# Performance work log

Hardware: AMD Instinct MI355X
Metric: run time of the kernel (lower is better)

Reference implementation:

```python
import jax, jax.numpy as jnp
import numpy as np
from jax import lax

B, N, CIN, COUT = 8, 4096, 64, 128
S, NS, V = 1024, 32, 4
RADIUS = 0.2
H1, H2 = 64, 128
BN_EPS = 1e-5


def _fps(xyz, n_sample):
    # farthest point sampling, deterministic start at index 0
    Bb, Nn, _ = xyz.shape
    start = jnp.zeros((Bb,), jnp.int32)
    mind0 = jnp.full((Bb, Nn), jnp.inf, xyz.dtype)

    def body(carry, _):
        mind, last = carry
        p = jnp.take_along_axis(xyz, last[:, None, None], axis=1)  # [B,1,3]
        d = jnp.sum((xyz - p) ** 2, -1)                             # [B,N]
        mind = jnp.minimum(mind, d)
        nxt = jnp.argmax(mind, -1).astype(jnp.int32)
        return (mind, nxt), nxt

    (_, _), rest = lax.scan(body, (mind0, start), None, length=n_sample - 1)
    idx = jnp.concatenate([start[None], rest], 0).T                 # [B,S]
    new_xyz = jnp.take_along_axis(xyz, idx[..., None], axis=1)      # [B,S,3]
    return new_xyz, idx


def _ball_query_idx(new_xyz, xyz, K, radius):
    # first K points (in index order) within radius, padded with -1
    d2 = jnp.sum((new_xyz[:, :, None, :] - xyz[:, None, :, :]) ** 2, -1)  # [B,S,N]
    within = d2 < radius * radius
    Nn = xyz.shape[1]
    ar = jnp.arange(Nn)
    key = jnp.where(within, ar, Nn + ar)            # in-ball points sort first, stably by index
    sel = jnp.argsort(key, axis=-1)[:, :, :K]       # [B,S,K]
    valid = jnp.take_along_axis(within, sel, axis=-1)
    return jnp.where(valid, sel, -1)


def _masked_gather(f, idx):
    # gather rows of f [B,N,C] with idx (any batched shape); idx==-1 -> zeros
    mask = idx == -1
    safe = jnp.where(mask, 0, idx)
    g = jax.vmap(lambda fb, ib: fb[ib])(f, safe)
    return jnp.where(mask[..., None], jnp.zeros((), f.dtype), g)


def _bn(x, gamma, beta, axes):
    # training-mode batchnorm over `axes` (channel is last dim)
    mu = jnp.mean(x, axes, keepdims=True)
    var = jnp.mean((x - mu) ** 2, axes, keepdims=True)
    return (x - mu) * (gamma / jnp.sqrt(var + BN_EPS)) + beta


def setup_inputs() -> dict:
    key = jax.random.key(0)
    ks = jax.random.split(key, 16)
    sc = 0.05
    inp = {
        "xyz": jax.random.uniform(ks[0], (B, N, 3), jnp.float32),
        "f": jax.random.normal(ks[1], (B, N, CIN), jnp.float32),
        "centroid_idx": jax.random.randint(ks[2], (V,), 0, NS),
        "affine_weight": jnp.ones((CIN + 6,), jnp.float32),
        "affine_bias": jnp.zeros((CIN + 6,), jnp.float32),
        "mix_w": sc * jax.random.normal(ks[3], (CIN, 2 * CIN + 6), jnp.float32),
        "mix_b": jnp.zeros((CIN,), jnp.float32),
        "m1_w1": sc * jax.random.normal(ks[4], (H1, 13), jnp.float32),
        "m1_b1": jnp.zeros((H1,), jnp.float32),
        "m1_g1": jnp.ones((H1,), jnp.float32),
        "m1_be1": jnp.zeros((H1,), jnp.float32),
        "m1_w2": sc * jax.random.normal(ks[5], (CIN, H1), jnp.float32),
        "m1_b2": jnp.zeros((CIN,), jnp.float32),
        "m2_w1": sc * jax.random.normal(ks[6], (H2, CIN), jnp.float32),
        "m2_b1": jnp.zeros((H2,), jnp.float32),
        "m2_g1": jnp.ones((H2,), jnp.float32),
        "m2_be1": jnp.zeros((H2,), jnp.float32),
        "m2_w2": sc * jax.random.normal(ks[7], (COUT, H2), jnp.float32),
        "m2_b2": jnp.zeros((COUT,), jnp.float32),
        "res_w": sc * jax.random.normal(ks[8], (COUT, CIN), jnp.float32),
        "res_b": jnp.zeros((COUT,), jnp.float32),
    }
    return inp


def reference(xyz, f, centroid_idx, affine_weight, affine_bias, mix_w, mix_b,
              m1_w1, m1_b1, m1_g1, m1_be1, m1_w2, m1_b2,
              m2_w1, m2_b1, m2_g1, m2_be1, m2_w2, m2_b2, res_w, res_b):
    Bb = xyz.shape[0]
    # ---- Grouping ----
    new_xyz, new_idx = _fps(xyz, S)                     # [B,S,3], [B,S]
    gidx = _ball_query_idx(new_xyz, xyz, NS, RADIUS)    # [B,S,n]
    mask = gidx == -1
    grouped_xyz = _masked_gather(xyz, gidx)             # [B,S,n,3]
    grouped_feat = _masked_gather(f, gidx)              # [B,S,n,cin]
    sampled = _masked_gather(f, new_idx)[:, :, None, :]  # [B,S,1,cin]
    gxl = grouped_xyz - new_xyz[:, :, None, :]
    gfl = grouped_feat - sampled
    gf = jnp.concatenate([grouped_xyz, gxl, gfl], -1)   # [B,S,n,cin+6]
    std = jnp.std(gf.reshape(Bb, -1), axis=-1, ddof=1).reshape(Bb, 1, 1, 1)
    gf = gf / (std + 1e-5)
    gf = affine_weight * gf + affine_bias
    gf = jnp.concatenate([gf, jnp.broadcast_to(sampled, (Bb, S, NS, CIN))], -1)
    grouped_f = jnp.einsum('bsnc,oc->bsno', gf, mix_w) + mix_b  # [B,S,n,cin]
    group_skip = grouped_f

    # ---- multi-centroid relative geometry (rel_jk, 13 channels) ----
    mc = xyz[:, centroid_idx, :]                                       # [B,V,3]
    arrow = grouped_xyz[:, :, :, None, :] - mc[:, None, None, :, :]    # [B,S,n,V,3]
    eu = jnp.sqrt(jnp.sum(arrow ** 2, -1, keepdims=True))              # [B,S,n,V,1]
    gx_b = jnp.broadcast_to(grouped_xyz[:, :, :, None, :], arrow.shape)
    mc_b = jnp.broadcast_to(mc[:, None, None, :, :], arrow.shape)
    rel = jnp.concatenate([-arrow, arrow, eu, gx_b, mc_b], -1)         # [B,S,n,V,13]

    # ---- m1: 1x1x1 Conv3d -> BN3d -> GELU -> Conv3d ----
    h = jnp.einsum('bsnvc,oc->bsnvo', rel, m1_w1) + m1_b1
    h = _bn(h, m1_g1, m1_be1, (0, 1, 2, 3))
    h = jax.nn.gelu(h, approximate=False)
    w_jk = jnp.einsum('bsnvc,oc->bsnvo', h, m1_w2) + m1_b2             # [B,S,n,V,cin]

    # ---- gumbel-softmax weighted aggregation over V centroids ----
    logits = grouped_f[:, :, :, None, :] * w_jk                        # [B,S,n,V,cin]
    u = jax.random.uniform(jax.random.key(42), logits.shape, logits.dtype, 1e-9, 1.0)
    gumbel = -jnp.log(-jnp.log(u))
    soft_w = jax.nn.softmax(logits + gumbel, axis=3)  # softmax over V (tau=1, soft)
    agg = jnp.sum(soft_w * logits, axis=3)                             # [B,S,n,cin]
    agg = agg + group_skip
    agg = jnp.where(mask[..., None], jnp.zeros((), agg.dtype), agg)

    # ---- m2: 1x1 Conv2d -> BN2d -> Conv2d, residual, max-pool over n ----
    h2 = jnp.einsum('bsnc,oc->bsno', agg, m2_w1) + m2_b1
    h2 = _bn(h2, m2_g1, m2_be1, (0, 1, 2))
    out = jnp.einsum('bsnc,oc->bsno', h2, m2_w2) + m2_b2               # [B,S,n,cout]
    res = jnp.einsum('bsnc,oc->bsno', group_skip, res_w) + res_b
    new_f = jax.nn.gelu(out + res, approximate=False)
    new_f = jnp.max(new_f, axis=2)                                     # [B,S,cout]
    return new_f, new_xyz
```

## Files before the change

kernel.cpp:

```cpp
#include <hip/hip_runtime.h>
#include <cstdint>
#include <cstddef>

#define TF_PARTITIONABLE 1

constexpr int B_ = 8, N_ = 4096, CIN_ = 64, COUT_ = 128;
constexpr int S_ = 1024, NS_ = 32, V_ = 4;
constexpr int ROWS_ = B_ * S_ * NS_;

constexpr size_t OFF_ACC   = 0;
constexpr size_t ACC_BYTES = 35072;
constexpr size_t OFF_SCALE = 35072;
constexpr size_t OFF_W1P   = 35328;
constexpr size_t OFF_B1P   = 38656;
constexpr size_t OFF_WCOMB = 38912;
constexpr size_t OFF_BCOMB = 71680;
constexpr size_t OFF_MIXWT = 72192;
constexpr size_t OFF_NIDX  = 106496;
constexpr size_t OFF_GIDX  = 139264;
constexpr size_t OFF_GF    = 1187840;
constexpr size_t OFF_AGG   = 68296704;

constexpr int AC_BATCH = 0;
constexpr int AC_G     = 16;
constexpr int AC_E     = 88;
constexpr int AC_S2A   = 216;
constexpr int AC_M2    = 280;

__device__ __forceinline__ float gelu_f(float x) {
    return 0.5f * x * (1.0f + erff(x * 0.7071067811865476f));
}

#define TF_ROUND(r) { x0 += x1; x1 = (x1 << (r)) | (x1 >> (32 - (r))); x1 ^= x0; }

__device__ __forceinline__ unsigned tf_random_bits(unsigned lo) {
    const unsigned ks0 = 0u, ks1 = 42u, ks2 = 0x1BD11BDAu ^ 0u ^ 42u;
#if TF_PARTITIONABLE
    unsigned x0 = 0u + ks0, x1 = lo + ks1;
#else
    unsigned j = lo & 0x01FFFFFFu;
    unsigned x0 = j + ks0, x1 = (j + 0x02000000u) + ks1;
#endif
    TF_ROUND(13) TF_ROUND(15) TF_ROUND(26) TF_ROUND(6)
    x0 += ks1; x1 += ks2 + 1u;
    TF_ROUND(17) TF_ROUND(29) TF_ROUND(16) TF_ROUND(24)
    x0 += ks2; x1 += ks0 + 2u;
    TF_ROUND(13) TF_ROUND(15) TF_ROUND(26) TF_ROUND(6)
    x0 += ks0; x1 += ks1 + 3u;
    TF_ROUND(17) TF_ROUND(29) TF_ROUND(16) TF_ROUND(24)
    x0 += ks1; x1 += ks2 + 4u;
    TF_ROUND(13) TF_ROUND(15) TF_ROUND(26) TF_ROUND(6)
    x0 += ks2; x1 += ks0 + 5u;
#if TF_PARTITIONABLE
    return x0 ^ x1;
#else
    return (lo < 0x02000000u) ? x0 : x1;
#endif
}

__device__ __forceinline__ float gumbel_from_bits(unsigned bits) {
    float fl = __uint_as_float((bits >> 9) | 0x3f800000u) - 1.0f;
    float u  = fmaxf(1e-9f, fl + 1e-9f);
    return -logf(-logf(u));
}

__device__ __forceinline__ float wsum(float v) {
    for (int o = 32; o; o >>= 1) v += __shfl_down(v, o);
    return v;
}

__global__ __launch_bounds__(256) void k_fps(const float* __restrict__ xyz,
                                             int* __restrict__ new_idx,
                                             float* __restrict__ new_xyz) {
    __shared__ float sx[4096], sy[4096], sz[4096];
    __shared__ __align__(16) float swv[2][4];
    __shared__ __align__(16) int   swi[2][4];
    int b = blockIdx.x, t = threadIdx.x, lane = t & 63, wid = t >> 6;
    const float* xb = xyz + (size_t)b * 12288;
    float px[16], py[16], pz[16], md[16];
    int i0 = t * 16;
#pragma unroll
    for (int j = 0; j < 16; j++) {
        int i = i0 + j;
        float x = xb[i * 3], y = xb[i * 3 + 1], z = xb[i * 3 + 2];
        px[j] = x; py[j] = y; pz[j] = z;
        sx[i] = x; sy[i] = y; sz[i] = z;
        md[j] = __builtin_inff();
    }
    __syncthreads();
    float cx = sx[0], cy = sy[0], cz = sz[0];
    if (t == 0) {
        new_idx[b * 1024] = 0;
        new_xyz[(size_t)b * 3072 + 0] = cx;
        new_xyz[(size_t)b * 3072 + 1] = cy;
        new_xyz[(size_t)b * 3072 + 2] = cz;
    }
    int p = 0;
    for (int it = 1; it < 1024; ++it) {
        float bv = -1.0f; int bj = 0;
#pragma unroll
        for (int j = 0; j < 16; j++) {
            float dx = __fsub_rn(px[j], cx), dy = __fsub_rn(py[j], cy), dz = __fsub_rn(pz[j], cz);
            float d = __fadd_rn(__fadd_rn(__fmul_rn(dx, dx), __fmul_rn(dy, dy)), __fmul_rn(dz, dz));
            float m2 = fminf(md[j], d); md[j] = m2;
            if (m2 > bv) { bv = m2; bj = j; }
        }
        int bi = i0 + bj;
        float mx = bv;
#pragma unroll
        for (int off = 1; off < 64; off <<= 1) mx = fmaxf(mx, __shfl_xor(mx, off));
        unsigned long long msk = __ballot(bv == mx);
        int winlane = __ffsll(msk) - 1;
        int wbi = __shfl(bi, winlane);
        if (lane == 0) { swv[p][wid] = mx; swi[p][wid] = wbi; }
        __syncthreads();
        float4 vv = *(const float4*)&swv[p][0];
        int4   ii4 = *(const int4*)&swi[p][0];
        float best = vv.x; int ii = ii4.x;
        if (vv.y > best) { best = vv.y; ii = ii4.y; }
        if (vv.z > best) { best = vv.z; ii = ii4.z; }
        if (vv.w > best) { best = vv.w; ii = ii4.w; }
        cx = sx[ii]; cy = sy[ii]; cz = sz[ii];
        if (t == 0) {
            new_idx[b * 1024 + it] = ii;
            size_t o3 = ((size_t)b * 1024 + it) * 3;
            new_xyz[o3] = cx; new_xyz[o3 + 1] = cy; new_xyz[o3 + 2] = cz;
        }
        p ^= 1;
    }
}

__global__ __launch_bounds__(256) void k_ball(const float* __restrict__ xyz,
                                              const float* __restrict__ new_xyz,
                                              int* __restrict__ gidx) {
    int gw = blockIdx.x * 4 + (threadIdx.x >> 6);
    int lane = threadIdx.x & 63;
    int b = gw >> 10;
    const float* xb = xyz + (size_t)b * 12288;
    float qx = new_xyz[gw * 3], qy = new_xyz[gw * 3 + 1], qz = new_xyz[gw * 3 + 2];
    int* out = gidx + (size_t)gw * 32;
    int have = 0;
    for (int c0 = 0; c0 < 4096; c0 += 64) {
        int i = c0 + lane;
        float dx = __fsub_rn(qx, xb[i * 3]);
        float dy = __fsub_rn(qy, xb[i * 3 + 1]);
        float dz = __fsub_rn(qz, xb[i * 3 + 2]);
        float d2 = __fadd_rn(__fadd_rn(__fmul_rn(dx, dx), __fmul_rn(dy, dy)), __fmul_rn(dz, dz));
        bool within = d2 < 0.04f;
        unsigned long long mv = __ballot(within);
        int rank = __popcll(mv & ((1ull << lane) - 1ull));
        int pos = have + rank;
        if (within && pos < 32) out[pos] = i;
        have += (int)__popcll(mv);
        if (have >= 32) break;
    }
    for (int j = have + lane; j < 32; j += 64) out[j] = -1;
}

__global__ __launch_bounds__(256) void k_stats(const float* __restrict__ xyz,
                                               const float* __restrict__ f,
                                               const int* __restrict__ cidx,
                                               const int* __restrict__ new_idx,
                                               const int* __restrict__ gidx,
                                               const float* __restrict__ new_xyz,
                                               double* __restrict__ acc) {
    int b = blockIdx.x >> 5, blk = blockIdx.x & 31;
    int t = threadIdx.x, lane = t & 63;
    const float* xb = xyz + (size_t)b * 12288;
    const float* fb = f + ((size_t)b << 18);
    float mc[4][3];
#pragma unroll
    for (int v = 0; v < 4; v++) {
        int ci = cidx[v];
        mc[v][0] = xb[ci * 3]; mc[v][1] = xb[ci * 3 + 1]; mc[v][2] = xb[ci * 3 + 2];
    }
    float sum = 0.f, ssq = 0.f;
    float G1x = 0, G1y = 0, G1z = 0, Gxx = 0, Gxy = 0, Gxz = 0, Gyy = 0, Gyz = 0, Gzz = 0;
    float E1[4] = {0, 0, 0, 0}, Eax[4] = {0, 0, 0, 0}, Eay[4] = {0, 0, 0, 0}, Eaz[4] = {0, 0, 0, 0};
    for (int rr = 0; rr < 4; ++rr) {
        int row = blk * 1024 + rr * 256 + t;
        int s = row >> 5;
        int gi = gidx[((size_t)b << 15) + row];
        bool msk = gi < 0;
        int sg = (b << 10) + s;
        float nx = new_xyz[sg * 3], ny = new_xyz[sg * 3 + 1], nz = new_xyz[sg * 3 + 2];
        int nid = new_idx[sg];
        float gx = 0, gy = 0, gz = 0;
        if (!msk) { gx = xb[gi * 3]; gy = xb[gi * 3 + 1]; gz = xb[gi * 3 + 2]; }
        float a3 = __fsub_rn(gx, nx), a4 = __fsub_rn(gy, ny), a5 = __fsub_rn(gz, nz);
        sum += gx + gy + gz + a3 + a4 + a5;
        ssq += gx * gx + gy * gy + gz * gz + a3 * a3 + a4 * a4 + a5 * a5;
        const float4* fsp = (const float4*)(fb + ((size_t)nid << 6));
        int gi0 = msk ? 0 : gi;
        const float4* fip = (const float4*)(fb + ((size_t)gi0 << 6));
#pragma unroll
        for (int c4 = 0; c4 < 16; c4++) {
            float4 fs4 = fsp[c4];
            float4 fi4 = fip[c4];
            if (msk) { fi4.x = 0; fi4.y = 0; fi4.z = 0; fi4.w = 0; }
            float d0 = __fsub_rn(fi4.x, fs4.x), d1 = __fsub_rn(fi4.y, fs4.y);
            float d2 = __fsub_rn(fi4.z, fs4.z), d3 = __fsub_rn(fi4.w, fs4.w);
            sum += d0 + d1 + d2 + d3;
            ssq += d0 * d0 + d1 * d1 + d2 * d2 + d3 * d3;
        }
        G1x += gx; G1y += gy; G1z += gz;
        Gxx += gx * gx; Gxy += gx * gy; Gxz += gx * gz;
        Gyy += gy * gy; Gyz += gy * gz; Gzz += gz * gz;
#pragma unroll
        for (int v = 0; v < 4; v++) {
            float ax = __fsub_rn(gx, mc[v][0]), ay = __fsub_rn(gy, mc[v][1]), az = __fsub_rn(gz, mc[v][2]);
            float e = __fsqrt_rn(ax * ax + ay * ay + az * az);
            E1[v] += e; Eax[v] += e * gx; Eay[v] += e * gy; Eaz[v] += e * gz;
        }
    }
    sum = wsum(sum); ssq = wsum(ssq);
    G1x = wsum(G1x); G1y = wsum(G1y); G1z = wsum(G1z);
    Gxx = wsum(Gxx); Gxy = wsum(Gxy); Gxz = wsum(Gxz);
    Gyy = wsum(Gyy); Gyz = wsum(Gyz); Gzz = wsum(Gzz);
#pragma unroll
    for (int v = 0; v < 4; v++) {
        E1[v] = wsum(E1[v]); Eax[v] = wsum(Eax[v]); Eay[v] = wsum(Eay[v]); Eaz[v] = wsum(Eaz[v]);
    }
    if (lane == 0) {
        atomicAdd(&acc[AC_BATCH + b * 2 + 0], (double)sum);
        atomicAdd(&acc[AC_BATCH + b * 2 + 1], (double)ssq);
        double* Gb = acc + AC_G + b * 9;
        atomicAdd(&Gb[0], (double)G1x); atomicAdd(&Gb[1], (double)G1y); atomicAdd(&Gb[2], (double)G1z);
        atomicAdd(&Gb[3], (double)Gxx); atomicAdd(&Gb[4], (double)Gxy); atomicAdd(&Gb[5], (double)Gxz);
        atomicAdd(&Gb[6], (double)Gyy); atomicAdd(&Gb[7], (double)Gyz); atomicAdd(&Gb[8], (double)Gzz);
#pragma unroll
        for (int v = 0; v < 4; v++) {
            double* Eb = acc + AC_E + (b * 4 + v) * 4;
            atomicAdd(&Eb[0], (double)E1[v]);
            atomicAdd(&Eb[1], (double)Eax[v]);
            atomicAdd(&Eb[2], (double)Eay[v]);
            atomicAdd(&Eb[3], (double)Eaz[v]);
        }
    }
}

struct GS { double G1[3]; double G2[6]; double E1; double Ea[3]; double m[3]; };

__device__ __forceinline__ int g2i(int x, int y) {
    if (x > y) { int tt = x; x = y; y = tt; }
    return (x == 0) ? y : ((x == 1) ? (2 + y) : 5);
}

__device__ double pairsum(const GS& g, int ki, int ai, int kj, int aj) {
    const double R = 32768.0;
    if (ki > kj) { int tk = ki; ki = kj; kj = tk; int ta = ai; ai = aj; aj = ta; }
    switch (ki * 4 + kj) {
        case 0:  return g.G2[g2i(ai, aj)] - g.m[ai] * g.G1[aj] - g.m[aj] * g.G1[ai] + R * g.m[ai] * g.m[aj];
        case 1:  return g.Ea[ai] - g.m[ai] * g.E1;
        case 2:  return g.G2[g2i(ai, aj)] - g.m[ai] * g.G1[aj];
        case 3:  return (g.G1[ai] - R * g.m[ai]) * g.m[aj];
        case 5:  { double s = 0; for (int x = 0; x < 3; x++) s += g.G2[g2i(x, x)] - 2.0 * g.m[x] * g.G1[x] + R * g.m[x] * g.m[x]; return s; }
        case 6:  return g.Ea[aj];
        case 7:  return g.E1 * g.m[aj];
        case 10: return g.G2[g2i(ai, aj)];
        case 11: return g.G1[ai] * g.m[aj];
        case 15: return R * g.m[ai] * g.m[aj];
    }
    return 0.0;
}

__device__ __forceinline__ void chdec(int ch, int& kind, int& ax, double& sgn) {
    if (ch < 3)      { kind = 0; ax = ch;      sgn = -1.0; }
    else if (ch < 6) { kind = 0; ax = ch - 3;  sgn = 1.0; }
    else if (ch == 6){ kind = 1; ax = 0;       sgn = 1.0; }
    else if (ch < 10){ kind = 2; ax = ch - 7;  sgn = 1.0; }
    else             { kind = 3; ax = ch - 10; sgn = 1.0; }
}

__device__ GS load_gs(const double* acc, const float* xyz, const int* cidx, int grp) {
    GS g; int b = grp >> 2, v = grp & 3;
    const double* Gb = acc + AC_G + b * 9;
    g.G1[0] = Gb[0]; g.G1[1] = Gb[1]; g.G1[2] = Gb[2];
    for (int q = 0; q < 6; q++) g.G2[q] = Gb[3 + q];
    const double* Eb = acc + AC_E + grp * 4;
    g.E1 = Eb[0]; g.Ea[0] = Eb[1]; g.Ea[1] = Eb[2]; g.Ea[2] = Eb[3];
    int ci = cidx[v];
    g.m[0] = (double)xyz[(size_t)b * 12288 + ci * 3];
    g.m[1] = (double)xyz[(size_t)b * 12288 + ci * 3 + 1];
    g.m[2] = (double)xyz[(size_t)b * 12288 + ci * 3 + 2];
    return g;
}

__global__ __launch_bounds__(256) void k_prep(const double* __restrict__ acc,
                                              const float* __restrict__ xyz,
                                              const int* __restrict__ cidx,
                                              const float* __restrict__ m1w1,
                                              const float* __restrict__ m1b1,
                                              const float* __restrict__ m1g1,
                                              const float* __restrict__ m1be1,
                                              const float* __restrict__ mixw,
                                              float* __restrict__ scale,
                                              float* __restrict__ w1p,
                                              float* __restrict__ b1p,
                                              float* __restrict__ mixwt) {
    __shared__ double Sec[169];
    __shared__ double S1[13];
    int t = threadIdx.x;
    if (t < 8) {
        double sm = acc[AC_BATCH + t * 2], sq = acc[AC_BATCH + t * 2 + 1];
        double M = 2293760.0;
        double var = (sq - sm * sm / M) / (M - 1.0);
        float stdv = (float)sqrt(var);
        scale[t] = 1.0f / (stdv + 1e-5f);
    }
    for (int idx = t; idx < 8576; idx += 256) {
        int k = idx >> 6, o = idx & 63;
        mixwt[idx] = mixw[o * 134 + k];
    }
    if (t < 169) {
        int i = t / 13, j = t % 13;
        int ki, ai, kj, aj; double si, sj;
        chdec(i, ki, ai, si); chdec(j, kj, aj, sj);
        double val = 0;
        for (int grp = 0; grp < 32; grp++) {
            GS g = load_gs(acc, xyz, cidx, grp);
            val += si * sj * pairsum(g, ki, ai, kj, aj);
        }
        Sec[t] = val;
    } else if (t < 182) {
        int i = t - 169;
        int ki, ai; double si;
        chdec(i, ki, ai, si);
        double val = 0;
        const double R = 32768.0;
        for (int grp = 0; grp < 32; grp++) {
            GS g = load_gs(acc, xyz, cidx, grp);
            double tv;
            switch (ki) {
                case 0:  tv = si * (g.G1[ai] - R * g.m[ai]); break;
                case 1:  tv = g.E1; break;
                case 2:  tv = g.G1[ai]; break;
                default: tv = R * g.m[ai]; break;
            }
            val += tv;
        }
        S1[i] = val;
    }
    __syncthreads();
    if (t < 64) {
        double w[13];
        for (int k = 0; k < 13; k++) w[k] = (double)m1w1[t * 13 + k];
        double s1w = 0;
        for (int k = 0; k < 13; k++) s1w += w[k] * S1[k];
        double quad = 0;
        for (int i = 0; i < 13; i++) {
            double s = 0;
            for (int j = 0; j < 13; j++) s += Sec[i * 13 + j] * w[j];
            quad += w[i] * s;
        }
        double M1d = 1048576.0;
        double b1o = (double)m1b1[t];
        double mu = s1w / M1d + b1o;
        double E2 = (quad + 2.0 * b1o * s1w) / M1d + b1o * b1o;
        double var = E2 - mu * mu;
        double gg = (double)m1g1[t] / sqrt(var + 1e-5);
        for (int k = 0; k < 13; k++) w1p[t * 13 + k] = (float)(w[k] * gg);
        b1p[t] = (float)((b1o - mu) * gg + (double)m1be1[t]);
    }
}

__global__ __launch_bounds__(256) void k_groupedf(const float* __restrict__ xyz,
                                                  const float* __restrict__ f,
                                                  const int* __restrict__ new_idx,
                                                  const int* __restrict__ gidx,
                                                  const float* __restrict__ new_xyz,
                                                  const float* __restrict__ scale_p,
                                                  const float* __restrict__ aw,
                                                  const float* __restrict__ ab,
                                                  const float* __restrict__ mixwt,
                                                  const float* __restrict__ mixb,
                                                  float* __restrict__ gf) {
    int r = blockIdx.x * 256 + threadIdx.x;
    int b = r >> 15;
    int rb = r & 32767;
    int s = rb >> 5;
    int gi = gidx[r];
    bool msk = gi < 0;
    int gi0 = msk ? 0 : gi;
    int sg = (b << 10) + s;
    int nid = new_idx[sg];
    float scale = scale_p[b];
    float nx = new_xyz[sg * 3], ny = new_xyz[sg * 3 + 1], nz = new_xyz[sg * 3 + 2];
    const float* xb = xyz + (size_t)b * 12288;
    const float* fb = f + ((size_t)b << 18);
    float gx = 0, gy = 0, gz = 0;
    if (!msk) { gx = xb[gi * 3]; gy = xb[gi * 3 + 1]; gz = xb[gi * 3 + 2]; }
    float acc[64];
#pragma unroll
    for (int o = 0; o < 64; o++) acc[o] = mixb[o];
    float va[6];
    va[0] = gx; va[1] = gy; va[2] = gz;
    va[3] = __fsub_rn(gx, nx); va[4] = __fsub_rn(gy, ny); va[5] = __fsub_rn(gz, nz);
#pragma unroll
    for (int k = 0; k < 6; k++) {
        float g = aw[k] * (va[k] * scale) + ab[k];
        const float* wt = mixwt + k * 64;
#pragma unroll
        for (int o = 0; o < 64; o++) acc[o] += g * wt[o];
    }
    const float4* fip = (const float4*)(fb + ((size_t)gi0 << 6));
    const float4* fsp = (const float4*)(fb + ((size_t)nid << 6));
    for (int c4 = 0; c4 < 16; c4++) {
        float4 fi = fip[c4];
        if (msk) { fi.x = 0; fi.y = 0; fi.z = 0; fi.w = 0; }
        float4 fs4 = fsp[c4];
        float dv[4] = {__fsub_rn(fi.x, fs4.x), __fsub_rn(fi.y, fs4.y),
                       __fsub_rn(fi.z, fs4.z), __fsub_rn(fi.w, fs4.w)};
#pragma unroll
        for (int u = 0; u < 4; u++) {
            int k = 6 + c4 * 4 + u;
            float g = aw[k] * (dv[u] * scale) + ab[k];
            const float* wt = mixwt + k * 64;
#pragma unroll
            for (int o = 0; o < 64; o++) acc[o] += g * wt[o];
        }
    }
    for (int c4 = 0; c4 < 16; c4++) {
        float4 fs4 = fsp[c4];
        float sv[4] = {fs4.x, fs4.y, fs4.z, fs4.w};
#pragma unroll
        for (int u = 0; u < 4; u++) {
            int k = 70 + c4 * 4 + u;
            const float* wt = mixwt + k * 64;
#pragma unroll
            for (int o = 0; o < 64; o++) acc[o] += sv[u] * wt[o];
        }
    }
    float4* dst = (float4*)(gf + ((size_t)r << 6));
#pragma unroll
    for (int c4 = 0; c4 < 16; c4++)
        dst[c4] = make_float4(acc[c4 * 4], acc[c4 * 4 + 1], acc[c4 * 4 + 2], acc[c4 * 4 + 3]);
}

__global__ __launch_bounds__(256) void k_fused(const float* __restrict__ xyz,
                                               const int* __restrict__ cidx,
                                               const int* __restrict__ gidx,
                                               const float* __restrict__ gf,
                                               const float* __restrict__ w1p,
                                               const float* __restrict__ b1p,
                                               const float* __restrict__ w2,
                                               const float* __restrict__ b2,
                                               float* __restrict__ agg) {
    __shared__ float sh[4][4][64];
    __shared__ float smc[4][3];
    int t = threadIdx.x, wv = t >> 6, lane = t & 63;
    int row0 = blockIdx.x * 64;
    int b = row0 >> 15;
    if (t < 12) {
        int v = t / 3, j = t % 3;
        smc[v][j] = xyz[(size_t)b * 12288 + cidx[v] * 3 + j];
    }
    float w1l[13];
#pragma unroll
    for (int k = 0; k < 13; k++) w1l[k] = w1p[lane * 13 + k];
    float b1l = b1p[lane], b2l = b2[lane];
    float w2r[64];
#pragma unroll
    for (int c4 = 0; c4 < 16; c4++) {
        float4 tmp = *(const float4*)(w2 + lane * 64 + c4 * 4);
        w2r[c4 * 4] = tmp.x; w2r[c4 * 4 + 1] = tmp.y; w2r[c4 * 4 + 2] = tmp.z; w2r[c4 * 4 + 3] = tmp.w;
    }
    __syncthreads();
    float mcl[4][3];
#pragma unroll
    for (int v = 0; v < 4; v++) { mcl[v][0] = smc[v][0]; mcl[v][1] = smc[v][1]; mcl[v][2] = smc[v][2]; }
    int r = row0 + wv * 16;
    for (int rr = 0; rr < 16; ++rr, ++r) {
        int gi = gidx[r];
        bool msk = gi < 0;
        float gx = 0, gy = 0, gz = 0;
        if (!msk) {
            const float* p = xyz + (size_t)b * 12288 + (size_t)gi * 3;
            gx = p[0]; gy = p[1]; gz = p[2];
        }
        float gfo = gf[((size_t)r << 6) + lane];
#pragma unroll
        for (int v = 0; v < 4; v++) {
            float ax = __fsub_rn(gx, mcl[v][0]);
            float ay = __fsub_rn(gy, mcl[v][1]);
            float az = __fsub_rn(gz, mcl[v][2]);
            float eu = __fsqrt_rn(__fadd_rn(__fadd_rn(__fmul_rn(ax, ax), __fmul_rn(ay, ay)), __fmul_rn(az, az)));
            float h = b1l
                - ax * w1l[0] - ay * w1l[1] - az * w1l[2]
                + ax * w1l[3] + ay * w1l[4] + az * w1l[5]
                + eu * w1l[6] + gx * w1l[7] + gy * w1l[8] + gz * w1l[9]
                + mcl[v][0] * w1l[10] + mcl[v][1] * w1l[11] + mcl[v][2] * w1l[12];
            sh[wv][v][lane] = gelu_f(h);
        }
        __syncthreads();
        float lg[4];
#pragma unroll
        for (int v = 0; v < 4; v++) {
            float a = b2l;
            const float4* hp = (const float4*)sh[wv][v];
#pragma unroll
            for (int c4 = 0; c4 < 16; c4++) {
                float4 hh = hp[c4];
                a += hh.x * w2r[c4 * 4] + hh.y * w2r[c4 * 4 + 1] + hh.z * w2r[c4 * 4 + 2] + hh.w * w2r[c4 * 4 + 3];
            }
            lg[v] = gfo * a;
        }
        __syncthreads();
        unsigned base = ((unsigned)r << 8) + (unsigned)lane;
        float z0 = lg[0] + gumbel_from_bits(tf_random_bits(base));
        float z1 = lg[1] + gumbel_from_bits(tf_random_bits(base + 64u));
        float z2 = lg[2] + gumbel_from_bits(tf_random_bits(base + 128u));
        float z3 = lg[3] + gumbel_from_bits(tf_random_bits(base + 192u));
        float mx = fmaxf(fmaxf(z0, z1), fmaxf(z2, z3));
        float e0 = __expf(z0 - mx), e1 = __expf(z1 - mx), e2 = __expf(z2 - mx), e3 = __expf(z3 - mx);
        float inv = 1.0f / (e0 + e1 + e2 + e3);
        float av = (e0 * lg[0] + e1 * lg[1] + e2 * lg[2] + e3 * lg[3]) * inv + gfo;
        agg[((size_t)r << 6) + lane] = msk ? 0.0f : av;
    }
}

__global__ __launch_bounds__(256) void k_syrk(const float* __restrict__ agg,
                                              double* __restrict__ acc) {
    __shared__ float As[128][64];
    int t = threadIdx.x;
    int ti = t >> 4, tj = t & 15;
    float C[4][4] = {};
    float cs = 0.f;
    size_t base = (size_t)blockIdx.x * 1024 * 64;
    for (int tile = 0; tile < 8; ++tile) {
        const float4* src = (const float4*)(agg + base + (size_t)tile * 128 * 64);
#pragma unroll
        for (int i = 0; i < 8; i++) {
            int idx = t + i * 256;
            ((float4*)As)[idx] = src[idx];
        }
        __syncthreads();
        for (int rr = 0; rr < 128; ++rr) {
            float4 a = *(const float4*)&As[rr][ti * 4];
            float4 bb = *(const float4*)&As[rr][tj * 4];
            C[0][0] += a.x * bb.x; C[0][1] += a.x * bb.y; C[0][2] += a.x * bb.z; C[0][3] += a.x * bb.w;
            C[1][0] += a.y * bb.x; C[1][1] += a.y * bb.y; C[1][2] += a.y * bb.z; C[1][3] += a.y * bb.w;
            C[2][0] += a.z * bb.x; C[2][1] += a.z * bb.y; C[2][2] += a.z * bb.z; C[2][3] += a.z * bb.w;
            C[3][0] += a.w * bb.x; C[3][1] += a.w * bb.y; C[3][2] += a.w * bb.z; C[3][3] += a.w * bb.w;
            if (t < 64) cs += As[rr][t];
        }
        __syncthreads();
    }
    double* M2 = acc + AC_M2;
#pragma unroll
    for (int i = 0; i < 4; i++)
#pragma unroll
        for (int j = 0; j < 4; j++)
            atomicAdd(&M2[(ti * 4 + i) * 64 + (tj * 4 + j)], (double)C[i][j]);
    if (t < 64) atomicAdd(&acc[AC_S2A + t], (double)cs);
}

__global__ __launch_bounds__(256) void k_comb(const double* __restrict__ acc,
                                              const float* __restrict__ m2w1,
                                              const float* __restrict__ m2b1,
                                              const float* __restrict__ m2g1,
                                              const float* __restrict__ m2be1,
                                              const float* __restrict__ m2w2,
                                              const float* __restrict__ m2b2,
                                              float* __restrict__ wcomb,
                                              float* __restrict__ bcomb) {
    __shared__ float W1s[128 * 64];
    __shared__ float g2s[128], ofss[128];
    int t = threadIdx.x;
    const double* S2a = acc + AC_S2A;
    const double* M2 = acc + AC_M2;
    if (t < 128) {
        float wf[64];
        for (int c = 0; c < 64; c++) wf[c] = m2w1[t * 64 + c];
        double sw = 0;
        for (int c = 0; c < 64; c++) sw += (double)wf[c] * S2a[c];
        double quad = 0;
        for (int i = 0; i < 64; i++) {
            double s = 0;
            for (int j = 0; j < 64; j++) s += (double)wf[j] * M2[i * 64 + j];
            quad += (double)wf[i] * s;
        }
        double Rd = 262144.0;
        double b1o = (double)m2b1[t];
        double mu = sw / Rd + b1o;
        double E2 = (quad + 2.0 * b1o * sw) / Rd + b1o * b1o;
        double var = E2 - mu * mu;
        double gg = (double)m2g1[t] / sqrt(var + 1e-5);
        g2s[t] = (float)gg;
        ofss[t] = (float)(((double)m2b1[t] - mu) * gg + (double)m2be1[t]);
    }
    __syncthreads();
    for (int idx = t; idx < 128 * 64; idx += 256) {
        int c = idx >> 6, k = idx & 63;
        W1s[idx] = g2s[c] * m2w1[c * 64 + k];
    }
    __syncthreads();
    for (int idx = t; idx < 128 * 64; idx += 256) {
        int o = idx >> 6, k = idx & 63;
        float s = 0;
        for (int c = 0; c < 128; c++) s += m2w2[o * 128 + c] * W1s[c * 64 + k];
        wcomb[idx] = s;
    }
    if (t < 128) {
        float s = m2b2[t];
        for (int c = 0; c < 128; c++) s += m2w2[t * 128 + c] * ofss[c];
        bcomb[t] = s;
    }
}

__global__ __launch_bounds__(256) void k_final(const float* __restrict__ agg,
                                               const float* __restrict__ gf,
                                               const float* __restrict__ wcomb,
                                               const float* __restrict__ bcomb,
                                               const float* __restrict__ resw,
                                               const float* __restrict__ resb,
                                               float* __restrict__ out_f) {
    __shared__ float rbuf[8][128];
    int t = threadIdx.x, wv = t >> 6, lane = t & 63;
    int which = lane >> 5, n = lane & 31;
    int gw = blockIdx.x * 8 + wv * 2 + which;
    size_t r = (size_t)gw * 32 + n;
    float ar[64], sk[64];
    const float4* ap = (const float4*)(agg + (r << 6));
    const float4* sp = (const float4*)(gf + (r << 6));
#pragma unroll
    for (int c4 = 0; c4 < 16; c4++) {
        float4 x = ap[c4];
        ar[c4 * 4] = x.x; ar[c4 * 4 + 1] = x.y; ar[c4 * 4 + 2] = x.z; ar[c4 * 4 + 3] = x.w;
        float4 y = sp[c4];
        sk[c4 * 4] = y.x; sk[c4 * 4 + 1] = y.y; sk[c4 * 4 + 2] = y.z; sk[c4 * 4 + 3] = y.w;
    }
    for (int o = 0; o < 128; o++) {
        float a1 = bcomb[o], a2 = resb[o];
        const float* wc = wcomb + o * 64;
        const float* rw = resw + o * 64;
#pragma unroll
        for (int c = 0; c < 64; c++) { a1 += ar[c] * wc[c]; a2 += sk[c] * rw[c]; }
        float g = gelu_f(a1 + a2);
#pragma unroll
        for (int off = 16; off; off >>= 1) g = fmaxf(g, __shfl_xor(g, off));
        if (n == 0) rbuf[wv * 2 + which][o] = g;
    }
    __syncthreads();
    int base = blockIdx.x * 8;
    for (int i = t; i < 1024; i += 256) {
        int lr = i >> 7, o = i & 127;
        out_f[(size_t)(base + lr) * 128 + o] = rbuf[lr][o];
    }
}

extern "C" void kernel_launch(void* const* d_in, const int* in_sizes, int n_in,
                              void* d_out, int out_size, void* d_ws, size_t ws_size,
                              hipStream_t stream) {
    (void)in_sizes; (void)n_in; (void)out_size; (void)ws_size;
    const float* xyz  = (const float*)d_in[0];
    const float* f    = (const float*)d_in[1];
    const int*   cidx = (const int*)d_in[2];
    const float* aw   = (const float*)d_in[3];
    const float* ab   = (const float*)d_in[4];
    const float* mixw = (const float*)d_in[5];
    const float* mixb = (const float*)d_in[6];
    const float* m1w1 = (const float*)d_in[7];
    const float* m1b1 = (const float*)d_in[8];
    const float* m1g1 = (const float*)d_in[9];
    const float* m1be1= (const float*)d_in[10];
    const float* m1w2 = (const float*)d_in[11];
    const float* m1b2 = (const float*)d_in[12];
    const float* m2w1 = (const float*)d_in[13];
    const float* m2b1 = (const float*)d_in[14];
    const float* m2g1 = (const float*)d_in[15];
    const float* m2be1= (const float*)d_in[16];
    const float* m2w2 = (const float*)d_in[17];
    const float* m2b2 = (const float*)d_in[18];
    const float* resw = (const float*)d_in[19];
    const float* resb = (const float*)d_in[20];

    float* out_f   = (float*)d_out;
    float* out_xyz = out_f + (size_t)B_ * S_ * COUT_;

    char* ws = (char*)d_ws;
    double* acc  = (double*)(ws + OFF_ACC);
    float* scale = (float*)(ws + OFF_SCALE);
    float* w1p   = (float*)(ws + OFF_W1P);
    float* b1p   = (float*)(ws + OFF_B1P);
    float* wcomb = (float*)(ws + OFF_WCOMB);
    float* bcomb = (float*)(ws + OFF_BCOMB);
    float* mixwt = (float*)(ws + OFF_MIXWT);
    int*   nidx  = (int*)(ws + OFF_NIDX);
    int*   gidx  = (int*)(ws + OFF_GIDX);
    float* gf    = (float*)(ws + OFF_GF);
    float* agg   = (float*)(ws + OFF_AGG);

    hipMemsetAsync(ws, 0, ACC_BYTES, stream);
    hipLaunchKernelGGL(k_fps,      dim3(8),    dim3(256),  0, stream, xyz, nidx, out_xyz);
    hipLaunchKernelGGL(k_ball,     dim3(2048), dim3(256),  0, stream, xyz, out_xyz, gidx);
    hipLaunchKernelGGL(k_stats,    dim3(256),  dim3(256),  0, stream, xyz, f, cidx, nidx, gidx, out_xyz, acc);
    hipLaunchKernelGGL(k_prep,     dim3(1),    dim3(256),  0, stream, acc, xyz, cidx, m1w1, m1b1, m1g1, m1be1, mixw, scale, w1p, b1p, mixwt);
    hipLaunchKernelGGL(k_groupedf, dim3(1024), dim3(256),  0, stream, xyz, f, nidx, gidx, out_xyz, scale, aw, ab, mixwt, mixb, gf);
    hipLaunchKernelGGL(k_fused,    dim3(4096), dim3(256),  0, stream, xyz, cidx, gidx, gf, w1p, b1p, m1w2, m1b2, agg);
    hipLaunchKernelGGL(k_syrk,     dim3(256),  dim3(256),  0, stream, agg, acc);
    hipLaunchKernelGGL(k_comb,     dim3(1),    dim3(256),  0, stream, acc, m2w1, m2b1, m2g1, m2be1, m2w2, m2b2, wcomb, bcomb);
    hipLaunchKernelGGL(k_final,    dim3(1024), dim3(256),  0, stream, agg, gf, wcomb, bcomb, resw, resb, out_f);
}
```

Before: 2.236 ms.

## Speed up FPS wave reduction with DPP, fast erf/log, drop block barriers

Several unrelated changes. The FPS argmax reduction now uses DPP row operations plus readlane instead of shfl_xor butterflies, and the point coordinates are packed into a float4 shared array so each centroid fetch is a single load. GELU uses a polynomial erf approximation (Abramowitz-Stegun), the outer log in the Gumbel noise uses __logf, and two __syncthreads in the per-row aggregation loop are removed because each wave only touches its own shared slice. The approximations may shift numerics, and dropping the barriers assumes no cross-wave sharing and relies on wave-level ordering for the LDS reuse.

```diff
diff --git a/kernel.cpp b/kernel.cpp
--- a/kernel.cpp
+++ b/kernel.cpp
@@ -27,8 +27,17 @@
 constexpr int AC_S2A   = 216;
 constexpr int AC_M2    = 280;
 
+__device__ __forceinline__ float erf_fast(float x) {
+    float ax = fabsf(x);
+    float t = 1.0f / (1.0f + 0.3275911f * ax);
+    float y = t * (0.254829592f + t * (-0.284496736f + t * (1.421413741f +
+              t * (-1.453152027f + t * 1.061405429f))));
+    float r = 1.0f - y * __expf(-ax * ax);
+    return copysignf(r, x);
+}
+
 __device__ __forceinline__ float gelu_f(float x) {
-    return 0.5f * x * (1.0f + erff(x * 0.7071067811865476f));
+    return 0.5f * x * (1.0f + erf_fast(x * 0.7071067811865476f));
 }
 
 #define TF_ROUND(r) { x0 += x1; x1 = (x1 << (r)) | (x1 >> (32 - (r))); x1 ^= x0; }
@@ -61,7 +70,8 @@
 __device__ __forceinline__ float gumbel_from_bits(unsigned bits) {
     float fl = __uint_as_float((bits >> 9) | 0x3f800000u) - 1.0f;
     float u  = fmaxf(1e-9f, fl + 1e-9f);
-    return -logf(-logf(u));
+    float w = -logf(u);
+    return -__logf(w);
 }
 
 __device__ __forceinline__ float wsum(float v) {
@@ -69,10 +79,27 @@
     return v;
 }
 
+__device__ __forceinline__ float wave_max64_nonneg(float v) {
+    int x;
+    x = __builtin_amdgcn_update_dpp(0, __float_as_int(v), 0xB1, 0xf, 0xf, true);
+    v = fmaxf(v, __int_as_float(x));
+    x = __builtin_amdgcn_update_dpp(0, __float_as_int(v), 0x4E, 0xf, 0xf, true);
+    v = fmaxf(v, __int_as_float(x));
+    x = __builtin_amdgcn_update_dpp(0, __float_as_int(v), 0x141, 0xf, 0xf, true);
+    v = fmaxf(v, __int_as_float(x));
+    x = __builtin_amdgcn_update_dpp(0, __float_as_int(v), 0x140, 0xf, 0xf, true);
+    v = fmaxf(v, __int_as_float(x));
+    x = __builtin_amdgcn_update_dpp(0, __float_as_int(v), 0x142, 0xf, 0xf, true);
+    v = fmaxf(v, __int_as_float(x));
+    x = __builtin_amdgcn_update_dpp(0, __float_as_int(v), 0x143, 0xf, 0xf, true);
+    v = fmaxf(v, __int_as_float(x));
+    return __int_as_float(__builtin_amdgcn_readlane(__float_as_int(v), 63));
+}
+
 __global__ __launch_bounds__(256) void k_fps(const float* __restrict__ xyz,
                                              int* __restrict__ new_idx,
                                              float* __restrict__ new_xyz) {
-    __shared__ float sx[4096], sy[4096], sz[4096];
+    __shared__ __align__(16) float4 sxyz[4096];
     __shared__ __align__(16) float swv[2][4];
     __shared__ __align__(16) int   swi[2][4];
     int b = blockIdx.x, t = threadIdx.x, lane = t & 63, wid = t >> 6;
@@ -84,11 +111,12 @@
         int i = i0 + j;
         float x = xb[i * 3], y = xb[i * 3 + 1], z = xb[i * 3 + 2];
         px[j] = x; py[j] = y; pz[j] = z;
-        sx[i] = x; sy[i] = y; sz[i] = z;
+        sxyz[i] = make_float4(x, y, z, 0.0f);
         md[j] = __builtin_inff();
     }
     __syncthreads();
-    float cx = sx[0], cy = sy[0], cz = sz[0];
+    float4 c0 = sxyz[0];
+    float cx = c0.x, cy = c0.y, cz = c0.z;
     if (t == 0) {
         new_idx[b * 1024] = 0;
         new_xyz[(size_t)b * 3072 + 0] = cx;
@@ -105,14 +133,10 @@
             float m2 = fminf(md[j], d); md[j] = m2;
             if (m2 > bv) { bv = m2; bj = j; }
         }
-        int bi = i0 + bj;
-        float mx = bv;
-#pragma unroll
-        for (int off = 1; off < 64; off <<= 1) mx = fmaxf(mx, __shfl_xor(mx, off));
+        float mx = wave_max64_nonneg(bv);
         unsigned long long msk = __ballot(bv == mx);
         int winlane = __ffsll(msk) - 1;
-        int wbi = __shfl(bi, winlane);
-        if (lane == 0) { swv[p][wid] = mx; swi[p][wid] = wbi; }
+        if (lane == winlane) { swv[p][wid] = bv; swi[p][wid] = i0 + bj; }
         __syncthreads();
         float4 vv = *(const float4*)&swv[p][0];
         int4   ii4 = *(const int4*)&swi[p][0];
@@ -120,7 +144,8 @@
         if (vv.y > best) { best = vv.y; ii = ii4.y; }
         if (vv.z > best) { best = vv.z; ii = ii4.z; }
         if (vv.w > best) { best = vv.w; ii = ii4.w; }
-        cx = sx[ii]; cy = sy[ii]; cz = sz[ii];
+        float4 cw = sxyz[ii];
+        cx = cw.x; cy = cw.y; cz = cw.z;
         if (t == 0) {
             new_idx[b * 1024 + it] = ii;
             size_t o3 = ((size_t)b * 1024 + it) * 3;
@@ -492,7 +517,6 @@
                 + mcl[v][0] * w1l[10] + mcl[v][1] * w1l[11] + mcl[v][2] * w1l[12];
             sh[wv][v][lane] = gelu_f(h);
         }
-        __syncthreads();
         float lg[4];
 #pragma unroll
         for (int v = 0; v < 4; v++) {
@@ -505,7 +529,6 @@
             }
             lg[v] = gfo * a;
         }
-        __syncthreads();
         unsigned base = ((unsigned)r << 8) + (unsigned)lane;
         float z0 = lg[0] + gumbel_from_bits(tf_random_bits(base));
         float z1 = lg[1] + gumbel_from_bits(tf_random_bits(base + 64u));
```

New measurement: 2.000 ms. 10.6% less time.
